# Performance work log

Hardware: AMD Instinct MI355X
Metric: run time of the kernel (lower is better)

## Reference

```python
import jax, jax.numpy as jnp
import numpy as np

N_HEAD = 16


def setup_inputs() -> dict:
    key = jax.random.key(0)
    ks = jax.random.split(key, 5)
    B, L, C = 2, 2048, 1024
    s = 0.02
    return {
        "x": jax.random.normal(ks[0], (B, L, C), dtype=jnp.float32),
        "attn_mask": jnp.ones((B, L), dtype=jnp.int64),
        "Wq": jax.random.normal(ks[1], (C, C), dtype=jnp.float32) * s,
        "Wk": jax.random.normal(ks[2], (C, C), dtype=jnp.float32) * s,
        "Wv": jax.random.normal(ks[3], (C, C), dtype=jnp.float32) * s,
        "Wp": jax.random.normal(ks[4], (C, C), dtype=jnp.float32) * s,
    }


def reference(x, attn_mask, Wq, Wk, Wv, Wp):
    B, L, C = x.shape
    H = N_HEAD
    D = C // H
    # nn.Linear(bias=False): y = x @ W.T with W of shape (out, in)
    q = (x @ Wq.T).reshape(B, L, H, D).transpose(0, 2, 1, 3)  # (B,H,L,D)
    k = (x @ Wk.T).reshape(B, L, H, D).transpose(0, 2, 1, 3)
    v = (x @ Wv.T).reshape(B, L, H, D).transpose(0, 2, 1, 3)
    att = jnp.einsum("bhqd,bhkd->bhqk", q, k) / jnp.sqrt(jnp.asarray(D, x.dtype))
    causal = jnp.tril(jnp.ones((L, L), dtype=bool))  # (L,L)
    tok = (attn_mask != 0)[:, None, None, :]  # (B,1,1,L) key-side padding mask
    mask = causal[None, None, :, :] & tok
    att = jnp.where(mask, att, -jnp.inf)
    att = jax.nn.softmax(att, axis=-1)
    # dropout p=0.0 (eval): identity
    y = jnp.einsum("bhqk,bhkd->bhqd", att, v)
    y = y.transpose(0, 2, 1, 3).reshape(B, L, C)
    return y @ Wp.T
```

## Files before the change

kernel.cpp:

```cpp
#include <hip/hip_runtime.h>
#include <hip/hip_bf16.h>
#include <cstdint>

typedef _Float16 f16;
typedef _Float16 f16x4 __attribute__((ext_vector_type(4)));
typedef _Float16 f16x8 __attribute__((ext_vector_type(8)));
typedef float f32x4 __attribute__((ext_vector_type(4)));

#define LNEG (-1e30f)

__device__ __forceinline__ f32x4 mfma16(f16x8 a, f16x8 b, f32x4 c){
    return __builtin_amdgcn_mfma_f32_16x16x32_f16(a, b, c, 0, 0, 0);
}

__global__ __launch_bounds__(256) void cvt5(
    const float* __restrict__ x,  const float* __restrict__ wq,
    const float* __restrict__ wk, const float* __restrict__ wv,
    const float* __restrict__ wp, f16* __restrict__ dst, int nx4, int nw4)
{
    int i = blockIdx.x * blockDim.x + threadIdx.x;
    const float* src; int off;
    if (i < nx4){ src = x; off = i; }
    else {
        int j = i - nx4;
        int s = j >> 18;
        off = j & (nw4 - 1);
        src = (s == 0) ? wq : (s == 1) ? wk : (s == 2) ? wv : wp;
    }
    float4 v = ((const float4*)src)[off];
    f16x4 o = { (f16)v.x, (f16)v.y, (f16)v.z, (f16)v.w };
    *(f16x4*)&dst[(size_t)i * 4] = o;
}

template<typename OutT>
__global__ __launch_bounds__(256) void gemm_xwt(
    const f16* __restrict__ A, const f16* __restrict__ W0, size_t wstride,
    OutT* __restrict__ out0, size_t ostride, int M, int N, int K)
{
    const int tid  = threadIdx.x;
    const int lane = tid & 63;
    const int w    = tid >> 6;
    const int wr   = w >> 1, wc = w & 1;
    const int m0   = blockIdx.y * 128;
    const int n0   = blockIdx.x * 128;
    const f16* Wz  = W0 + wstride * blockIdx.z;
    OutT* out      = out0 + ostride * blockIdx.z;

    __shared__ f16 At[2][128 * 64];
    __shared__ f16 Bt[2][128 * 64];

    f32x4 acc[4][4] = {};
    f16x8 avr[4], bvr[4];

    int srow[4], scolb[4], sswz[4];
    #pragma unroll
    for (int j = 0; j < 4; ++j){
        int off  = (j * 256 + tid) * 16;
        srow[j]  = off >> 7;
        scolb[j] = off & 127;
        sswz[j]  = srow[j] * 128 + (scolb[j] ^ ((srow[j] & 7) << 4));
    }

    #pragma unroll
    for (int j = 0; j < 4; ++j){
        avr[j] = *(const f16x8*)&A [(size_t)(m0 + srow[j]) * K + (scolb[j] >> 1)];
        bvr[j] = *(const f16x8*)&Wz[(size_t)(n0 + srow[j]) * K + (scolb[j] >> 1)];
    }
    #pragma unroll
    for (int j = 0; j < 4; ++j){
        *(f16x8*)((char*)At[0] + sswz[j]) = avr[j];
        *(f16x8*)((char*)Bt[0] + sswz[j]) = bvr[j];
    }
    __syncthreads();

    const int NT = K >> 6;
    for (int t = 0; t < NT; ++t){
        const int cur = t & 1;
        const bool pre = (t + 1 < NT);
        if (pre){
            const int k0 = (t + 1) << 6;
            #pragma unroll
            for (int j = 0; j < 4; ++j){
                avr[j] = *(const f16x8*)&A [(size_t)(m0 + srow[j]) * K + k0 + (scolb[j] >> 1)];
                bvr[j] = *(const f16x8*)&Wz[(size_t)(n0 + srow[j]) * K + k0 + (scolb[j] >> 1)];
            }
        }
        #pragma unroll
        for (int kk = 0; kk < 2; ++kk){
            f16x8 af[4], bf[4];
            #pragma unroll
            for (int mf = 0; mf < 4; ++mf){
                int row = wr * 64 + mf * 16 + (lane & 15);
                int cb  = (kk * 64 + 16 * (lane >> 4)) ^ ((row & 7) << 4);
                af[mf] = *(const f16x8*)((const char*)At[cur] + row * 128 + cb);
            }
            #pragma unroll
            for (int nf = 0; nf < 4; ++nf){
                int row = wc * 64 + nf * 16 + (lane & 15);
                int cb  = (kk * 64 + 16 * (lane >> 4)) ^ ((row & 7) << 4);
                bf[nf] = *(const f16x8*)((const char*)Bt[cur] + row * 128 + cb);
            }
            #pragma unroll
            for (int mf = 0; mf < 4; ++mf)
                #pragma unroll
                for (int nf = 0; nf < 4; ++nf)
                    acc[mf][nf] = mfma16(af[mf], bf[nf], acc[mf][nf]);
        }
        if (pre){
            const int nb = cur ^ 1;
            #pragma unroll
            for (int j = 0; j < 4; ++j){
                *(f16x8*)((char*)At[nb] + sswz[j]) = avr[j];
                *(f16x8*)((char*)Bt[nb] + sswz[j]) = bvr[j];
            }
        }
        __syncthreads();
    }
    #pragma unroll
    for (int mf = 0; mf < 4; ++mf)
        #pragma unroll
        for (int nf = 0; nf < 4; ++nf)
            #pragma unroll
            for (int r = 0; r < 4; ++r){
                int row = m0 + wr * 64 + mf * 16 + 4 * (lane >> 4) + r;
                int col = n0 + wc * 64 + nf * 16 + (lane & 15);
                out[(size_t)row * N + col] = (OutT)acc[mf][nf][r];
            }
}

__global__ __launch_bounds__(256) void transpose_v(const f16* __restrict__ v, f16* __restrict__ vt){
    const int t  = threadIdx.x;
    const int lt = blockIdx.x;
    const int bh = blockIdx.y;
    const int b  = bh >> 4, h = bh & 15;
    const int l0 = lt * 64;
    __shared__ f16 tile[64][72];
    #pragma unroll
    for (int r = 0; r < 2; ++r){
        int i  = t / 8 + 32 * r;
        int jb = t % 8;
        f16x8 vv = *(const f16x8*)&v[(size_t)(b * 2048 + l0 + i) * 1024 + h * 64 + jb * 8];
        *(f16x8*)&tile[i][jb * 8] = vv;
    }
    __syncthreads();
    #pragma unroll
    for (int r = 0; r < 2; ++r){
        int d  = t / 8 + 32 * r;
        int lb = t % 8;
        f16x8 o;
        #pragma unroll
        for (int q2 = 0; q2 < 8; ++q2) o[q2] = tile[lb * 8 + q2][d];
        *(f16x8*)&vt[(size_t)(bh * 64 + d) * 2048 + l0 + lb * 8] = o;
    }
}

__global__ __launch_bounds__(256, 4) void attn_fused(
    const f16* __restrict__ q, const f16* __restrict__ k,
    const f16* __restrict__ vt, const int* __restrict__ amask,
    f16* __restrict__ y)
{
    const int tid  = threadIdx.x;
    const int lane = tid & 63;
    const int w    = tid >> 6;
    const int g    = lane >> 4;
    const int qq   = lane & 15;

    const int lin = blockIdx.x;
    const int bh  = ((lin & 7) << 2) | ((lin >> 3) & 3);
    const int qtv = (lin >> 5) & 31;
    const int q5  = (qtv & 7) | ((qtv & 16) >> 1);
    const int qt  = (qtv & 8) ? (31 - q5) : q5;
    const int b = bh >> 4, h = bh & 15;
    const int q0w = qt * 64 + w * 16;
    const int nkt = qt + 1;

    __shared__ char sK[2][64 * 128];
    __shared__ char sV[2][64 * 128];
    __shared__ char sP[4][16 * 128];

    const int srow = (tid * 2) >> 3;
    const int sc8a = (tid * 2) & 7, sc8b = sc8a + 1;
    const int swka = (sc8a * 16) ^ ((srow & 7) << 4);
    const int swkb = (sc8b * 16) ^ ((srow & 7) << 4);
    const f16* kbase  = k  + ((size_t)b * 2048) * 1024 + h * 64;
    const f16* vtbase = vt + (size_t)bh * 64 * 2048;

    const f16 qscale = (f16)(0.125f * 1.44269504088896f);
    f16x8 aq[2];
    #pragma unroll
    for (int f = 0; f < 2; ++f){
        aq[f] = *(const f16x8*)&q[((size_t)(b * 2048 + q0w + qq)) * 1024 + h * 64 + f * 32 + 8 * g];
        #pragma unroll
        for (int j = 0; j < 8; ++j) aq[f][j] *= qscale;
    }

    f32x4 acc_o[4] = {};
    float m_ln = LNEG, l_ln = 0.f;

    char* pbase = sP[w] + qq * 128;
    const int swp = (qq & 7) << 4;

    {
        f16x8 ka  = *(const f16x8*)(kbase  + (size_t)srow * 1024 + sc8a * 8);
        f16x8 kb2 = *(const f16x8*)(kbase  + (size_t)srow * 1024 + sc8b * 8);
        f16x8 va  = *(const f16x8*)(vtbase + (size_t)srow * 2048 + sc8a * 8);
        f16x8 vb  = *(const f16x8*)(vtbase + (size_t)srow * 2048 + sc8b * 8);
        *(f16x8*)(sK[0] + srow * 128 + swka) = ka;
        *(f16x8*)(sK[0] + srow * 128 + swkb) = kb2;
        *(f16x8*)(sV[0] + srow * 128 + swka) = va;
        *(f16x8*)(sV[0] + srow * 128 + swkb) = vb;
    }
    __syncthreads();

    for (int kt = 0; kt < nkt; ++kt){
        const int cur = kt & 1;
        const int k0 = kt * 64;
        const bool pre = (kt + 1 < nkt);

        f16x8 ka, kb2, va, vb;
        if (pre){
            const int nk0 = k0 + 64;
            ka  = *(const f16x8*)(kbase  + (size_t)(nk0 + srow) * 1024 + sc8a * 8);
            kb2 = *(const f16x8*)(kbase  + (size_t)(nk0 + srow) * 1024 + sc8b * 8);
            va  = *(const f16x8*)(vtbase + (size_t)srow * 2048 + nk0 + sc8a * 8);
            vb  = *(const f16x8*)(vtbase + (size_t)srow * 2048 + nk0 + sc8b * 8);
        }

        unsigned long long tokbits = __ballot(amask[b * 2048 + k0 + lane] != 0);
        const bool tokall = (tokbits == ~0ull);

        f32x4 acc_s[4] = {};
        #pragma unroll
        for (int kf = 0; kf < 4; ++kf){
            const int keyl = kf * 16 + qq;
            const char* kr = sK[cur] + keyl * 128;
            const int sw = (keyl & 7) << 4;
            #pragma unroll
            for (int f = 0; f < 2; ++f){
                f16x8 ak = *(const f16x8*)(kr + ((f * 64 + 16 * g) ^ sw));
                acc_s[kf] = mfma16(ak, aq[f], acc_s[kf]);
            }
        }

        const bool fullt = (k0 + 63 <= q0w) && tokall;
        float sv[16];
        #pragma unroll
        for (int kf = 0; kf < 4; ++kf)
            #pragma unroll
            for (int r = 0; r < 4; ++r){
                float s = acc_s[kf][r];
                if (!fullt){
                    const int keyl = kf * 16 + 4 * g + r;
                    const bool ok = (k0 + keyl <= q0w + qq) && ((tokbits >> keyl) & 1);
                    s = ok ? s : LNEG;
                }
                sv[kf * 4 + r] = s;
            }

        float tmax = sv[0];
        #pragma unroll
        for (int i = 1; i < 16; ++i) tmax = fmaxf(tmax, sv[i]);
        tmax = fmaxf(tmax, __shfl_xor(tmax, 16));
        tmax = fmaxf(tmax, __shfl_xor(tmax, 32));
        const bool skip = __all(tmax <= m_ln + 8.f);
        float alpha = 1.f;
        if (!skip){
            const float newm = fmaxf(m_ln, tmax);
            alpha = exp2f(m_ln - newm);
            m_ln = newm;
        }
        float rs = 0.f;
        #pragma unroll
        for (int i = 0; i < 16; ++i){ sv[i] = exp2f(sv[i] - m_ln); rs += sv[i]; }
        rs += __shfl_xor(rs, 16);
        rs += __shfl_xor(rs, 32);
        l_ln = l_ln * alpha + rs;
        if (!skip){
            #pragma unroll
            for (int r = 0; r < 4; ++r){
                const float ar = __shfl(alpha, 4 * g + r);
                #pragma unroll
                for (int nf = 0; nf < 4; ++nf) acc_o[nf][r] *= ar;
            }
        }

        #pragma unroll
        for (int kf = 0; kf < 4; ++kf){
            f16x4 pk = { (f16)sv[kf*4+0], (f16)sv[kf*4+1], (f16)sv[kf*4+2], (f16)sv[kf*4+3] };
            *(f16x4*)(pbase + ((kf * 32 + 8 * g) ^ swp)) = pk;
        }
        __builtin_amdgcn_wave_barrier();

        #pragma unroll
        for (int f = 0; f < 2; ++f){
            f16x8 ap = *(const f16x8*)(pbase + ((f * 64 + 16 * g) ^ swp));
            #pragma unroll
            for (int nf = 0; nf < 4; ++nf){
                const int d = nf * 16 + qq;
                f16x8 bv = *(const f16x8*)(sV[cur] + d * 128 + ((f * 64 + 16 * g) ^ ((d & 7) << 4)));
                acc_o[nf] = mfma16(ap, bv, acc_o[nf]);
            }
        }
        __builtin_amdgcn_wave_barrier();

        if (pre){
            const int nb = cur ^ 1;
            *(f16x8*)(sK[nb] + srow * 128 + swka) = ka;
            *(f16x8*)(sK[nb] + srow * 128 + swkb) = kb2;
            *(f16x8*)(sV[nb] + srow * 128 + swka) = va;
            *(f16x8*)(sV[nb] + srow * 128 + swkb) = vb;
        }
        __syncthreads();
    }

    const float invl = 1.f / l_ln;
    #pragma unroll
    for (int r = 0; r < 4; ++r){
        const float ir = __shfl(invl, 4 * g + r);
        const int row = q0w + 4 * g + r;
        #pragma unroll
        for (int nf = 0; nf < 4; ++nf)
            y[((size_t)(b * 2048 + row)) * 1024 + h * 64 + nf * 16 + qq] = (f16)(acc_o[nf][r] * ir);
    }
}

extern "C" void kernel_launch(void* const* d_in, const int* in_sizes, int n_in,
                              void* d_out, int out_size, void* d_ws, size_t ws_size,
                              hipStream_t stream){
    const float* x  = (const float*)d_in[0];
    const int*   am = (const int*)d_in[1];
    const float* Wq = (const float*)d_in[2];
    const float* Wk = (const float*)d_in[3];
    const float* Wv = (const float*)d_in[4];
    const float* Wp = (const float*)d_in[5];
    float* out = (float*)d_out;

    char* ws = (char*)d_ws;
    const size_t XE = (size_t)4096 * 1024;
    const size_t WE = (size_t)1024 * 1024;

    f16* x16 = (f16*)(ws);
    f16* w16 = (f16*)(ws + XE * 2);
    f16* qkv = (f16*)(ws + XE * 2 + WE * 8);
    f16* vt  = (f16*)(ws + XE * 2 + WE * 8 + XE * 6);
    f16* y16 = (f16*)(ws + XE * 2 + WE * 8 + XE * 8);

    cvt5<<<8192, 256, 0, stream>>>(x, Wq, Wk, Wv, Wp, x16,
                                   (int)(XE / 4), (int)(WE / 4));

    gemm_xwt<f16><<<dim3(8, 32, 3), 256, 0, stream>>>(x16, w16, WE, qkv, XE, 4096, 1024, 1024);

    transpose_v<<<dim3(32, 32), 256, 0, stream>>>(qkv + 2 * XE, vt);

    attn_fused<<<dim3(1024), 256, 0, stream>>>(qkv, qkv + XE, vt, am, y16);

    gemm_xwt<float><<<dim3(8, 32, 1), 256, 0, stream>>>(y16, w16 + 3 * WE, 0, out, 0, 4096, 1024, 1024);
}
```

Before: 126.6 us.

## Fuse V transpose into QKV GEMM epilogue and use native exp2

The QKV projection GEMM now writes the V slice directly in transposed (bh, d, l) layout from its epilogue, which removes the separate transpose_v kernel launch and its extra read and write of V. Each lane stores four consecutive sequence positions as one 8-byte vector, so the stores are strided across rows and less coalesced than before. Separately, the softmax exponentials switch from exp2f to the raw hardware exp2 builtin to skip library range handling.

Result: faster. 114.1 us (-9.9%).

```diff
diff --git a/kernel.cpp b/kernel.cpp
--- a/kernel.cpp
+++ b/kernel.cpp
@@ -8,6 +8,7 @@
 typedef float f32x4 __attribute__((ext_vector_type(4)));
 
 #define LNEG (-1e30f)
+#define EXP2(x) __builtin_amdgcn_exp2f(x)
 
 __device__ __forceinline__ f32x4 mfma16(f16x8 a, f16x8 b, f32x4 c){
     return __builtin_amdgcn_mfma_f32_16x16x32_f16(a, b, c, 0, 0, 0);
@@ -35,7 +36,8 @@
 template<typename OutT>
 __global__ __launch_bounds__(256) void gemm_xwt(
     const f16* __restrict__ A, const f16* __restrict__ W0, size_t wstride,
-    OutT* __restrict__ out0, size_t ostride, int M, int N, int K)
+    OutT* __restrict__ out0, size_t ostride, f16* __restrict__ vtout,
+    int M, int N, int K)
 {
     const int tid  = threadIdx.x;
     const int lane = tid & 63;
@@ -116,41 +118,31 @@
         }
         __syncthreads();
     }
-    #pragma unroll
-    for (int mf = 0; mf < 4; ++mf)
-        #pragma unroll
-        for (int nf = 0; nf < 4; ++nf)
-            #pragma unroll
-            for (int r = 0; r < 4; ++r){
-                int row = m0 + wr * 64 + mf * 16 + 4 * (lane >> 4) + r;
+
+    if (vtout != nullptr && blockIdx.z == 2){
+        #pragma unroll
+        for (int mf = 0; mf < 4; ++mf)
+            #pragma unroll
+            for (int nf = 0; nf < 4; ++nf){
+                int row = m0 + wr * 64 + mf * 16 + 4 * (lane >> 4);
                 int col = n0 + wc * 64 + nf * 16 + (lane & 15);
-                out[(size_t)row * N + col] = (OutT)acc[mf][nf][r];
-            }
-}
-
-__global__ __launch_bounds__(256) void transpose_v(const f16* __restrict__ v, f16* __restrict__ vt){
-    const int t  = threadIdx.x;
-    const int lt = blockIdx.x;
-    const int bh = blockIdx.y;
-    const int b  = bh >> 4, h = bh & 15;
-    const int l0 = lt * 64;
-    __shared__ f16 tile[64][72];
-    #pragma unroll
-    for (int r = 0; r < 2; ++r){
-        int i  = t / 8 + 32 * r;
-        int jb = t % 8;
-        f16x8 vv = *(const f16x8*)&v[(size_t)(b * 2048 + l0 + i) * 1024 + h * 64 + jb * 8];
-        *(f16x8*)&tile[i][jb * 8] = vv;
-    }
-    __syncthreads();
-    #pragma unroll
-    for (int r = 0; r < 2; ++r){
-        int d  = t / 8 + 32 * r;
-        int lb = t % 8;
-        f16x8 o;
-        #pragma unroll
-        for (int q2 = 0; q2 < 8; ++q2) o[q2] = tile[lb * 8 + q2][d];
-        *(f16x8*)&vt[(size_t)(bh * 64 + d) * 2048 + l0 + lb * 8] = o;
+                int bb = row >> 11, ll = row & 2047;
+                int bh = bb * 16 + (col >> 6), dd = col & 63;
+                f16x4 o = { (f16)acc[mf][nf][0], (f16)acc[mf][nf][1],
+                            (f16)acc[mf][nf][2], (f16)acc[mf][nf][3] };
+                *(f16x4*)&vtout[((size_t)(bh * 64 + dd)) * 2048 + ll] = o;
+            }
+    } else {
+        #pragma unroll
+        for (int mf = 0; mf < 4; ++mf)
+            #pragma unroll
+            for (int nf = 0; nf < 4; ++nf)
+                #pragma unroll
+                for (int r = 0; r < 4; ++r){
+                    int row = m0 + wr * 64 + mf * 16 + 4 * (lane >> 4) + r;
+                    int col = n0 + wc * 64 + nf * 16 + (lane & 15);
+                    out[(size_t)row * N + col] = (OutT)acc[mf][nf][r];
+                }
     }
 }
 
@@ -266,12 +258,12 @@
         float alpha = 1.f;
         if (!skip){
             const float newm = fmaxf(m_ln, tmax);
-            alpha = exp2f(m_ln - newm);
+            alpha = EXP2(m_ln - newm);
             m_ln = newm;
         }
         float rs = 0.f;
         #pragma unroll
-        for (int i = 0; i < 16; ++i){ sv[i] = exp2f(sv[i] - m_ln); rs += sv[i]; }
+        for (int i = 0; i < 16; ++i){ sv[i] = EXP2(sv[i] - m_ln); rs += sv[i]; }
         rs += __shfl_xor(rs, 16);
         rs += __shfl_xor(rs, 32);
         l_ln = l_ln * alpha + rs;
@@ -348,11 +340,9 @@
     cvt5<<<8192, 256, 0, stream>>>(x, Wq, Wk, Wv, Wp, x16,
                                    (int)(XE / 4), (int)(WE / 4));
 
-    gemm_xwt<f16><<<dim3(8, 32, 3), 256, 0, stream>>>(x16, w16, WE, qkv, XE, 4096, 1024, 1024);
-
-    transpose_v<<<dim3(32, 32), 256, 0, stream>>>(qkv + 2 * XE, vt);
+    gemm_xwt<f16><<<dim3(8, 32, 3), 256, 0, stream>>>(x16, w16, WE, qkv, XE, vt, 4096, 1024, 1024);
 
     attn_fused<<<dim3(1024), 256, 0, stream>>>(qkv, qkv + XE, vt, am, y16);
 
-    gemm_xwt<float><<<dim3(8, 32, 1), 256, 0, stream>>>(y16, w16 + 3 * WE, 0, out, 0, 4096, 1024, 1024);
-}
+    gemm_xwt<float><<<dim3(8, 32, 1), 256, 0, stream>>>(y16, w16 + 3 * WE, 0, out, 0, nullptr, 4096, 1024, 1024);
+}
```
